# Optimization experiments

Hardware: AMD Instinct MI355X
Metric: run time of the kernel (lower is better)

Reference implementation:

```python
import jax, jax.numpy as jnp
import numpy as np

B, S = 8, 1024
D_MODEL = 1024
N_HEAD, HEAD_DIM = 16, 64
FIELD_W, FIELD_H = 32, 32  # S must equal FIELD_W * FIELD_H


def rotate_half(x):
    x1, x2 = jnp.split(x, 2, axis=-1)
    return jnp.concatenate((-x2, x1), axis=-1)


def apply_rope(q, k, cos, sin):
    # q,k: [B,S,H,D]; cos,sin: [S,D] -> broadcast over heads
    c = cos[:, None, :]
    s = sin[:, None, :]
    return q * c + rotate_half(q) * s, k * c + rotate_half(k) * s


def attention(q, k, v):
    # q,k,v: [B,S,H,D]; returns [B,S,H,D]
    scores = jnp.einsum('bqhd,bkhd->bhqk', q, k) * (HEAD_DIM ** -0.5)
    p = jax.nn.softmax(scores, axis=-1)
    return jnp.einsum('bhqk,bkhd->bqhd', p, v)


def setup_inputs() -> dict:
    key = jax.random.key(0)
    ks = jax.random.split(key, 5)
    hidden_states = jax.random.normal(ks[0], (B, S, D_MODEL), jnp.float32)
    cos = jax.random.uniform(ks[1], (S, HEAD_DIM), jnp.float32, minval=-1.0, maxval=1.0)
    sin = jax.random.uniform(ks[2], (S, HEAD_DIM), jnp.float32, minval=-1.0, maxval=1.0)
    w_qkv = jax.random.normal(ks[3], (3 * N_HEAD * HEAD_DIM, D_MODEL), jnp.float32) * (D_MODEL ** -0.5)
    w_o = jax.random.normal(ks[4], (D_MODEL, N_HEAD * HEAD_DIM), jnp.float32) * ((N_HEAD * HEAD_DIM) ** -0.5)
    return {"hidden_states": hidden_states, "cos": cos, "sin": sin, "w_qkv": w_qkv, "w_o": w_o}


def reference(hidden_states, cos, sin, w_qkv, w_o):
    b, s, _ = hidden_states.shape
    qkv = hidden_states @ w_qkv.T                       # [B,S,3*H*D]
    qkv = qkv.reshape(b, s, 3 * N_HEAD, HEAD_DIM)
    q = qkv[:, :, :N_HEAD]
    k = qkv[:, :, N_HEAD:2 * N_HEAD]
    v = qkv[:, :, 2 * N_HEAD:]
    # horizontal pass: standard RoPE
    q1, k1 = apply_rope(q, k, cos[:s], sin[:s])
    attn_out = attention(q1, k1, v)
    # vertical pass: transposed-field RoPE indexing
    idx = jnp.arange(FIELD_W * FIELD_H).reshape(FIELD_W, FIELD_H).T.reshape(-1)
    q2, k2 = apply_rope(q, k, cos[idx], sin[idx])
    attn_out_v = attention(q2, k2, v)
    attn_out = (attn_out + attn_out_v) * 0.5
    return attn_out.reshape(b, s, N_HEAD * HEAD_DIM) @ w_o.T
```

## Files before the change

kernel.cpp:

```cpp
#include <hip/hip_runtime.h>


typedef __attribute__((ext_vector_type(8))) short s16x8;
typedef __attribute__((ext_vector_type(4))) float f32x4;
typedef __attribute__((ext_vector_type(16))) float f32x16;
typedef unsigned short ushort_t;

__device__ __forceinline__ float bf2f(unsigned short u) {
    unsigned x = ((unsigned)u) << 16;
    return __builtin_bit_cast(float, x);
}
__device__ __forceinline__ unsigned short f2bf(float f) {
    unsigned u = __builtin_bit_cast(unsigned, f);
    unsigned r = (u + 0x7fffu + ((u >> 16) & 1u)) >> 16;
    return (unsigned short)r;
}
__device__ __forceinline__ f32x4 mfma16(s16x8 a, s16x8 b, f32x4 c) {
    return __builtin_amdgcn_mfma_f32_16x16x32_bf16(a, b, c, 0, 0, 0);
}
__device__ __forceinline__ f32x16 mfma32(s16x8 a, s16x8 b, f32x16 c) {
    return __builtin_amdgcn_mfma_f32_32x32x16_bf16(a, b, c, 0, 0, 0);
}
__device__ __forceinline__ void gload16(const ushort_t* g, ushort_t* lds) {
    __builtin_amdgcn_global_load_lds(
        (const __attribute__((address_space(1))) unsigned int*)g,
        (__attribute__((address_space(3))) unsigned int*)lds, 16, 0, 0);
}
__device__ __forceinline__ float4 ld4f(const float* p) { return *reinterpret_cast<const float4*>(p); }
__device__ __forceinline__ s16x8 ldg8(const ushort_t* p) { return *reinterpret_cast<const s16x8*>(p); }

__device__ __forceinline__ unsigned cvtpk(float lo, float hi) {
    unsigned r;
    asm("v_cvt_pk_bf16_f32 %0, %1, %2" : "=v"(r) : "v"(lo), "v"(hi));
    return r;
}
__device__ __forceinline__ void pl32swap(unsigned& a, unsigned& b, int hi) {
#if __has_builtin(__builtin_amdgcn_permlane32_swap)
    auto r = __builtin_amdgcn_permlane32_swap((int)a, (int)b, false, false);
    a = (unsigned)r[0]; b = (unsigned)r[1];
#else
    unsigned sa = (unsigned)__shfl_xor((int)a, 32);
    unsigned sb = (unsigned)__shfl_xor((int)b, 32);
    unsigned na = hi ? sb : a;
    unsigned nb = hi ? b : sa;
    a = na; b = nb;
#endif
}
__device__ __forceinline__ s16x8 frag4(unsigned w0, unsigned w1, unsigned w2, unsigned w3) {
    union { unsigned u[4]; s16x8 v; } t;
    t.u[0] = w0; t.u[1] = w1; t.u[2] = w2; t.u[3] = w3;
    return t.v;
}

__global__ __launch_bounds__(256) void conv_f32_bf16(const float* __restrict__ s,
                                                     ushort_t* __restrict__ d, int n8)
{
    int i = blockIdx.x * blockDim.x + threadIdx.x;
    const int str = gridDim.x * blockDim.x;
    for (; i < n8; i += str) {
        float4 a = ld4f(s + (size_t)i * 8);
        float4 b = ld4f(s + (size_t)i * 8 + 4);
        s16x8 o;
        o[0] = (short)f2bf(a.x); o[1] = (short)f2bf(a.y); o[2] = (short)f2bf(a.z); o[3] = (short)f2bf(a.w);
        o[4] = (short)f2bf(b.x); o[5] = (short)f2bf(b.y); o[6] = (short)f2bf(b.z); o[7] = (short)f2bf(b.w);
        *reinterpret_cast<s16x8*>(d + (size_t)i * 8) = o;
    }
}

__global__ __launch_bounds__(256) void avg_to_bf16(const float* __restrict__ a,
                                                   const float* __restrict__ b,
                                                   ushort_t* __restrict__ o, int n8)
{
    int i = blockIdx.x * blockDim.x + threadIdx.x;
    const int str = gridDim.x * blockDim.x;
    for (; i < n8; i += str) {
        float4 x0 = ld4f(a + (size_t)i * 8), x1 = ld4f(a + (size_t)i * 8 + 4);
        float4 y0 = ld4f(b + (size_t)i * 8), y1 = ld4f(b + (size_t)i * 8 + 4);
        s16x8 v;
        v[0] = (short)f2bf(0.5f * (x0.x + y0.x)); v[1] = (short)f2bf(0.5f * (x0.y + y0.y));
        v[2] = (short)f2bf(0.5f * (x0.z + y0.z)); v[3] = (short)f2bf(0.5f * (x0.w + y0.w));
        v[4] = (short)f2bf(0.5f * (x1.x + y1.x)); v[5] = (short)f2bf(0.5f * (x1.y + y1.y));
        v[6] = (short)f2bf(0.5f * (x1.z + y1.z)); v[7] = (short)f2bf(0.5f * (x1.w + y1.w));
        *reinterpret_cast<s16x8*>(o + (size_t)i * 8) = v;
    }
}

template<bool SPLIT_QKV>
__global__ __launch_bounds__(256) void gemm_mfma(const ushort_t* __restrict__ A,
                                                 const ushort_t* __restrict__ B,
                                                 void* __restrict__ C0, void* __restrict__ C1,
                                                 void* __restrict__ C2,
                                                 int M, int N, int K)
{
    __shared__ ushort_t As[128 * 64];
    __shared__ ushort_t Bs[128 * 64];
    const int tid = threadIdx.x, l = tid & 63, w = tid >> 6;
    const int lr = l & 15, lg = l >> 4;
    const int m0 = blockIdx.y * 128, n0 = blockIdx.x * 128;
    const int wr = w >> 1, wc = w & 1;

    int srow[4], scol[4];
#pragma unroll
    for (int i = 0; i < 4; ++i) {
        const int chunk = i * 4 + w;
        const int row = chunk * 8 + (l >> 3);
        srow[i] = row;
        scol[i] = ((l & 7) ^ (row & 7)) * 8;
    }

    f32x4 acc[4][4];
#pragma unroll
    for (int mi = 0; mi < 4; ++mi)
#pragma unroll
        for (int ni = 0; ni < 4; ++ni) acc[mi][ni] = (f32x4){0.f, 0.f, 0.f, 0.f};

    for (int k0 = 0; k0 < K; k0 += 64) {
        __syncthreads();
#pragma unroll
        for (int i = 0; i < 4; ++i) {
            gload16(A + (size_t)(m0 + srow[i]) * K + k0 + scol[i], &As[(i * 4 + w) * 512]);
            gload16(B + (size_t)(n0 + srow[i]) * K + k0 + scol[i], &Bs[(i * 4 + w) * 512]);
        }
        __syncthreads();
#pragma unroll
        for (int kf = 0; kf < 2; ++kf) {
            s16x8 af[4], bf[4];
#pragma unroll
            for (int mi = 0; mi < 4; ++mi) {
                const int row = wr * 64 + mi * 16 + lr;
                af[mi] = *reinterpret_cast<const s16x8*>(&As[row * 64 + (((kf * 4 + lg) ^ (row & 7)) << 3)]);
            }
#pragma unroll
            for (int ni = 0; ni < 4; ++ni) {
                const int row = wc * 64 + ni * 16 + lr;
                bf[ni] = *reinterpret_cast<const s16x8*>(&Bs[row * 64 + (((kf * 4 + lg) ^ (row & 7)) << 3)]);
            }
#pragma unroll
            for (int mi = 0; mi < 4; ++mi)
#pragma unroll
                for (int ni = 0; ni < 4; ++ni)
                    acc[mi][ni] = mfma16(af[mi], bf[ni], acc[mi][ni]);
        }
    }

    if (SPLIT_QKV) {
        ushort_t* Cb = (ushort_t*)(n0 < 1024 ? C0 : (n0 < 2048 ? C1 : C2));
        const int nbase = n0 & 1023;
#pragma unroll
        for (int mi = 0; mi < 4; ++mi)
#pragma unroll
            for (int q = 0; q < 4; ++q) {
                const int row = m0 + wr * 64 + mi * 16 + lg * 4 + q;
#pragma unroll
                for (int ni = 0; ni < 4; ++ni)
                    Cb[(size_t)row * 1024 + nbase + wc * 64 + ni * 16 + lr] = f2bf(acc[mi][ni][q]);
            }
    } else {
#pragma unroll
        for (int mi = 0; mi < 4; ++mi)
#pragma unroll
            for (int q = 0; q < 4; ++q) {
                const int row = m0 + wr * 64 + mi * 16 + lg * 4 + q;
#pragma unroll
                for (int ni = 0; ni < 4; ++ni)
                    ((float*)C0)[(size_t)row * N + n0 + wc * 64 + ni * 16 + lr] = acc[mi][ni][q];
            }
    }
}

__global__ __launch_bounds__(256) void rope_rearrange(
    const ushort_t* __restrict__ kb, const ushort_t* __restrict__ vb,
    const float* __restrict__ cosp, const float* __restrict__ sinp,
    ushort_t* __restrict__ Kr, ushort_t* __restrict__ Vt)
{
    __shared__ ushort_t Vs[64 * 65];
    const int tid = threadIdx.x;
    const int sblk = blockIdx.x, h = blockIdx.y, b = blockIdx.z;
    const int r = tid >> 2, c16 = (tid & 3) * 16;
    const int cc = c16 ^ 32;
    const float sg = (c16 < 32) ? -1.f : 1.f;
    const int s = sblk * 64 + r;

    const ushort_t* krow = kb + (size_t)(b * 1024 + s) * 1024 + h * 64;
    const ushort_t* vrow = vb + (size_t)(b * 1024 + s) * 1024 + h * 64;

    s16x8 kx0 = ldg8(krow + c16), kx1 = ldg8(krow + c16 + 8);
    s16x8 ky0 = ldg8(krow + cc),  ky1 = ldg8(krow + cc + 8);

#pragma unroll
    for (int var = 0; var < 2; ++var) {
        const int pos = var ? ((s & 31) * 32 + (s >> 5)) : s;
        const float* crow = cosp + (size_t)pos * 64 + c16;
        const float* srow = sinp + (size_t)pos * 64 + c16;
        ushort_t* kout = Kr + (((size_t)(var * 8 + b) * 16 + h) * 1024 + s) * 64 + c16;
        s16x8 o0, o1;
#pragma unroll
        for (int j = 0; j < 8; ++j) {
            o0[j] = (short)f2bf(bf2f((unsigned short)kx0[j]) * crow[j]
                     + sg * bf2f((unsigned short)ky0[j]) * srow[j]);
            o1[j] = (short)f2bf(bf2f((unsigned short)kx1[j]) * crow[j + 8]
                     + sg * bf2f((unsigned short)ky1[j]) * srow[j + 8]);
        }
        *reinterpret_cast<s16x8*>(kout) = o0;
        *reinterpret_cast<s16x8*>(kout + 8) = o1;
    }

    s16x8 v0 = ldg8(vrow + c16), v1 = ldg8(vrow + c16 + 8);
#pragma unroll
    for (int j = 0; j < 8; ++j) {
        Vs[r * 65 + c16 + j] = (ushort_t)v0[j];
        Vs[r * 65 + c16 + 8 + j] = (ushort_t)v1[j];
    }
    __syncthreads();
    {
        const int dd = tid >> 2, cs = (tid & 3) * 16;
        s16x8 t0, t1;
#pragma unroll
        for (int j = 0; j < 8; ++j) {
            t0[j] = (short)Vs[(cs + j) * 65 + dd];
            t1[j] = (short)Vs[(cs + 8 + j) * 65 + dd];
        }
        ushort_t* vout = Vt + ((size_t)(b * 16 + h) * 64 + dd) * 1024 + sblk * 64 + cs;
        *reinterpret_cast<s16x8*>(vout) = t0;
        *reinterpret_cast<s16x8*>(vout + 8) = t1;
    }
}

__global__ __launch_bounds__(256) void attn_mfma4(
    const ushort_t* __restrict__ qb,
    const ushort_t* __restrict__ Kr,
    const ushort_t* __restrict__ Vt,
    const float* __restrict__ cosp, const float* __restrict__ sinp,
    float* __restrict__ out0, float* __restrict__ out1)
{
    __shared__ ushort_t Qs[128 * 64];
    __shared__ ushort_t Ks[64 * 64];
    __shared__ ushort_t Vs[64 * 64];

    const int bi = blockIdx.x;
    const int qt = (bi >> 3) & 7;
    const int g = ((bi >> 6) << 3) | (bi & 7);
    const int h = g & 15, bz = g >> 4;
    const int b = bz >> 1, var = bz & 1;

    const int tid = threadIdx.x;
    const int l = tid & 63, wq = tid >> 6;
    const int l31 = l & 31, hi = l >> 5;
    const int s0 = qt * 128;

    {
        const int r = tid >> 1;
        const int half = tid & 1;
        const int c32 = half * 32, cco = 32 - c32;
        const float sg = half ? 1.f : -1.f;
        const int p = s0 + r;
        const int pos = var ? ((p & 31) * 32 + (p >> 5)) : p;
        const ushort_t* qrow = qb + (size_t)(b * 1024 + p) * 1024 + h * 64;
        const float* crow = cosp + (size_t)pos * 64 + c32;
        const float* srow = sinp + (size_t)pos * 64 + c32;
        constexpr float SCALE = 0.125f * 1.44269504f;
#pragma unroll
        for (int u = 0; u < 4; ++u) {
            s16x8 xv = ldg8(qrow + c32 + u * 8);
            s16x8 yv = ldg8(qrow + cco + u * 8);
            s16x8 ov;
#pragma unroll
            for (int j = 0; j < 8; ++j) {
                const int e = u * 8 + j;
                ov[j] = (short)f2bf((bf2f((unsigned short)xv[j]) * crow[e]
                         + sg * bf2f((unsigned short)yv[j]) * srow[e]) * SCALE);
            }
            const int slot = ((c32 >> 3) + u) ^ (r & 7);
            *reinterpret_cast<s16x8*>(&Qs[r * 64 + slot * 8]) = ov;
        }
    }
    __syncthreads();

    s16x8 qf[4];
    {
        const int qrow = wq * 32 + l31;
#pragma unroll
        for (int kc = 0; kc < 4; ++kc)
            qf[kc] = *reinterpret_cast<const s16x8*>(
                &Qs[qrow * 64 + (((2 * kc + hi) ^ (qrow & 7)) << 3)]);
    }

    float l_i = 0.f;
    f32x16 O0, O1;
#pragma unroll
    for (int r = 0; r < 16; ++r) { O0[r] = 0.f; O1[r] = 0.f; }

    const ushort_t* kr_base = Kr + ((size_t)(var * 8 + b) * 16 + h) * 65536;
    const ushort_t* vt_base = Vt + ((size_t)(b * 16 + h)) * 65536;
    const int lrow8 = l >> 3;
    const int scol = ((l & 7) ^ lrow8) * 8;

    for (int kt = 0; kt < 16; ++kt) {
        __syncthreads();
#pragma unroll
        for (int i = 0; i < 2; ++i) {
            const int chunk = wq * 2 + i;
            const int row = chunk * 8 + lrow8;
            gload16(kr_base + (size_t)kt * 4096 + row * 64 + scol, &Ks[chunk * 512]);
            gload16(vt_base + (size_t)row * 1024 + kt * 64 + scol, &Vs[chunk * 512]);
        }
        __syncthreads();

        f32x16 St0, St1;
#pragma unroll
        for (int r = 0; r < 16; ++r) { St0[r] = 0.f; St1[r] = 0.f; }
        const int kr0 = l31, kr1 = 32 + l31;
#pragma unroll
        for (int kc = 0; kc < 4; ++kc) {
            s16x8 kf0 = *reinterpret_cast<const s16x8*>(
                &Ks[kr0 * 64 + (((2 * kc + hi) ^ (kr0 & 7)) << 3)]);
            s16x8 kf1 = *reinterpret_cast<const s16x8*>(
                &Ks[kr1 * 64 + (((2 * kc + hi) ^ (kr1 & 7)) << 3)]);
            St0 = mfma32(kf0, qf[kc], St0);
            St1 = mfma32(kf1, qf[kc], St1);
        }

        float rs0 = 0.f, rs1 = 0.f;
#pragma unroll
        for (int r = 0; r < 16; ++r) { St0[r] = __builtin_amdgcn_exp2f(St0[r]); rs0 += St0[r]; }
#pragma unroll
        for (int r = 0; r < 16; ++r) { St1[r] = __builtin_amdgcn_exp2f(St1[r]); rs1 += St1[r]; }
        l_i += rs0 + rs1;

#pragma unroll
        for (int t = 0; t < 2; ++t) {
            unsigned w0, w1, w2, w3, w4, w5, w6, w7;
            if (t == 0) {
                w0 = cvtpk(St0[0], St0[1]);   w1 = cvtpk(St0[2], St0[3]);
                w2 = cvtpk(St0[4], St0[5]);   w3 = cvtpk(St0[6], St0[7]);
                w4 = cvtpk(St0[8], St0[9]);   w5 = cvtpk(St0[10], St0[11]);
                w6 = cvtpk(St0[12], St0[13]); w7 = cvtpk(St0[14], St0[15]);
            } else {
                w0 = cvtpk(St1[0], St1[1]);   w1 = cvtpk(St1[2], St1[3]);
                w2 = cvtpk(St1[4], St1[5]);   w3 = cvtpk(St1[6], St1[7]);
                w4 = cvtpk(St1[8], St1[9]);   w5 = cvtpk(St1[10], St1[11]);
                w6 = cvtpk(St1[12], St1[13]); w7 = cvtpk(St1[14], St1[15]);
            }
            pl32swap(w0, w2, hi);
            pl32swap(w1, w3, hi);
            pl32swap(w4, w6, hi);
            pl32swap(w5, w7, hi);
            const s16x8 pf0 = frag4(w0, w1, w2, w3);
            const s16x8 pf1 = frag4(w4, w5, w6, w7);
#pragma unroll
            for (int cc = 0; cc < 2; ++cc) {
                const int c = 2 * t + cc;
                const s16x8 pf = cc ? pf1 : pf0;
                const int vr0 = l31, vr1 = 32 + l31;
                s16x8 vf0 = *reinterpret_cast<const s16x8*>(
                    &Vs[vr0 * 64 + (((2 * c + hi) ^ (vr0 & 7)) << 3)]);
                s16x8 vf1 = *reinterpret_cast<const s16x8*>(
                    &Vs[vr1 * 64 + (((2 * c + hi) ^ (vr1 & 7)) << 3)]);
                O0 = mfma32(vf0, pf, O0);
                O1 = mfma32(vf1, pf, O1);
            }
        }
    }

    float* outp = var ? out1 : out0;
    const float inv = 1.f / (l_i + __shfl_xor(l_i, 32));
    const int qrow = s0 + wq * 32 + l31;
    float* orow = outp + (size_t)(b * 1024 + qrow) * 1024 + h * 64;
#pragma unroll
    for (int gq = 0; gq < 4; ++gq) {
        const int d0 = 8 * gq + 4 * hi;
        *reinterpret_cast<float4*>(orow + d0) =
            make_float4(O0[4 * gq] * inv, O0[4 * gq + 1] * inv, O0[4 * gq + 2] * inv, O0[4 * gq + 3] * inv);
        *reinterpret_cast<float4*>(orow + 32 + d0) =
            make_float4(O1[4 * gq] * inv, O1[4 * gq + 1] * inv, O1[4 * gq + 2] * inv, O1[4 * gq + 3] * inv);
    }
}

extern "C" void kernel_launch(void* const* d_in, const int* in_sizes, int n_in,
                              void* d_out, int out_size, void* d_ws, size_t ws_size,
                              hipStream_t stream) {
    const float* hidden = (const float*)d_in[0];
    const float* cosp   = (const float*)d_in[1];
    const float* sinp   = (const float*)d_in[2];
    const float* wqkv   = (const float*)d_in[3];
    const float* wo     = (const float*)d_in[4];
    float* out = (float*)d_out;

    char* wsb = (char*)d_ws;
    ushort_t* hb      = (ushort_t*)(wsb);
    ushort_t* wqkvb   = (ushort_t*)(wsb + (16ull << 20));
    ushort_t* wob     = (ushort_t*)(wsb + (22ull << 20));
    ushort_t* qb      = (ushort_t*)(wsb + (24ull << 20));
    ushort_t* kb      = (ushort_t*)(wsb + (40ull << 20));
    ushort_t* vb      = (ushort_t*)(wsb + (56ull << 20));
    float*    attn0   = (float*)   (wsb + (40ull << 20));
    ushort_t* Kr      = (ushort_t*)(wsb + (72ull << 20));
    ushort_t* Vt      = hb;
    ushort_t* attnavg = (ushort_t*)(wsb + (104ull << 20));

    conv_f32_bf16<<<2048, 256, 0, stream>>>(hidden, hb, 8192 * 1024 / 8);
    conv_f32_bf16<<<768,  256, 0, stream>>>(wqkv, wqkvb, 3072 * 1024 / 8);
    conv_f32_bf16<<<256,  256, 0, stream>>>(wo, wob, 1024 * 1024 / 8);

    gemm_mfma<true><<<dim3(24, 64), 256, 0, stream>>>(hb, wqkvb, qb, kb, vb, 8192, 3072, 1024);

    rope_rearrange<<<dim3(16, 16, 8), 256, 0, stream>>>(kb, vb, cosp, sinp, Kr, Vt);

    attn_mfma4<<<2048, 256, 0, stream>>>(qb, Kr, Vt, cosp, sinp, attn0, out);

    avg_to_bf16<<<2048, 256, 0, stream>>>(attn0, out, attnavg, 8192 * 1024 / 8);

    gemm_mfma<false><<<dim3(8, 64), 256, 0, stream>>>(attnavg, wob, out, nullptr, nullptr, 8192, 1024, 1024);
}
```

Measured before the change: 323.1 us.

## Fuse both RoPE attention variants per block and average into bf16 in-kernel

The attention kernel now processes both RoPE variants (horizontal and transposed) in one block, accumulating the two normalized outputs with a 0.5 weight and writing a single bf16 averaged tensor. This removes the two fp32 attention output writes, the separate averaging kernel and its reads. The three fp32-to-bf16 conversion launches are merged into one kernel. In exchange, the grid halves to 1024 blocks, each with twice the serial work, which lowers parallelism and keeps extra accumulator registers live.

Measured after the change: 378.9 us. 1.17x slower.

```diff
diff --git a/kernel.cpp b/kernel.cpp
--- a/kernel.cpp
+++ b/kernel.cpp
@@ -4,6 +4,7 @@
 typedef __attribute__((ext_vector_type(8))) short s16x8;
 typedef __attribute__((ext_vector_type(4))) float f32x4;
 typedef __attribute__((ext_vector_type(16))) float f32x16;
+typedef __attribute__((ext_vector_type(2))) unsigned u32x2;
 typedef unsigned short ushort_t;
 
 __device__ __forceinline__ float bf2f(unsigned short u) {
@@ -52,36 +53,25 @@
     return t.v;
 }
 
-__global__ __launch_bounds__(256) void conv_f32_bf16(const float* __restrict__ s,
-                                                     ushort_t* __restrict__ d, int n8)
+__global__ __launch_bounds__(256) void conv3(
+    const float* __restrict__ sA, ushort_t* __restrict__ dA, int nA,
+    const float* __restrict__ sB, ushort_t* __restrict__ dB, int nB,
+    const float* __restrict__ sC, ushort_t* __restrict__ dC, int nC)
 {
+    const int total = nA + nB + nC;
     int i = blockIdx.x * blockDim.x + threadIdx.x;
     const int str = gridDim.x * blockDim.x;
-    for (; i < n8; i += str) {
-        float4 a = ld4f(s + (size_t)i * 8);
-        float4 b = ld4f(s + (size_t)i * 8 + 4);
+    for (; i < total; i += str) {
+        const float* s; ushort_t* d; int off;
+        if (i < nA)           { s = sA; d = dA; off = i; }
+        else if (i < nA + nB) { s = sB; d = dB; off = i - nA; }
+        else                  { s = sC; d = dC; off = i - nA - nB; }
+        float4 a = ld4f(s + (size_t)off * 8);
+        float4 b = ld4f(s + (size_t)off * 8 + 4);
         s16x8 o;
         o[0] = (short)f2bf(a.x); o[1] = (short)f2bf(a.y); o[2] = (short)f2bf(a.z); o[3] = (short)f2bf(a.w);
         o[4] = (short)f2bf(b.x); o[5] = (short)f2bf(b.y); o[6] = (short)f2bf(b.z); o[7] = (short)f2bf(b.w);
-        *reinterpret_cast<s16x8*>(d + (size_t)i * 8) = o;
-    }
-}
-
-__global__ __launch_bounds__(256) void avg_to_bf16(const float* __restrict__ a,
-                                                   const float* __restrict__ b,
-                                                   ushort_t* __restrict__ o, int n8)
-{
-    int i = blockIdx.x * blockDim.x + threadIdx.x;
-    const int str = gridDim.x * blockDim.x;
-    for (; i < n8; i += str) {
-        float4 x0 = ld4f(a + (size_t)i * 8), x1 = ld4f(a + (size_t)i * 8 + 4);
-        float4 y0 = ld4f(b + (size_t)i * 8), y1 = ld4f(b + (size_t)i * 8 + 4);
-        s16x8 v;
-        v[0] = (short)f2bf(0.5f * (x0.x + y0.x)); v[1] = (short)f2bf(0.5f * (x0.y + y0.y));
-        v[2] = (short)f2bf(0.5f * (x0.z + y0.z)); v[3] = (short)f2bf(0.5f * (x0.w + y0.w));
-        v[4] = (short)f2bf(0.5f * (x1.x + y1.x)); v[5] = (short)f2bf(0.5f * (x1.y + y1.y));
-        v[6] = (short)f2bf(0.5f * (x1.z + y1.z)); v[7] = (short)f2bf(0.5f * (x1.w + y1.w));
-        *reinterpret_cast<s16x8*>(o + (size_t)i * 8) = v;
+        *reinterpret_cast<s16x8*>(d + (size_t)off * 8) = o;
     }
 }
 
@@ -226,12 +216,12 @@
     }
 }
 
-__global__ __launch_bounds__(256) void attn_mfma4(
+__global__ __launch_bounds__(256) void attn_mfma5(
     const ushort_t* __restrict__ qb,
     const ushort_t* __restrict__ Kr,
     const ushort_t* __restrict__ Vt,
     const float* __restrict__ cosp, const float* __restrict__ sinp,
-    float* __restrict__ out0, float* __restrict__ out1)
+    ushort_t* __restrict__ outavg)
 {
     __shared__ ushort_t Qs[128 * 64];
     __shared__ ushort_t Ks[64 * 64];
@@ -240,139 +230,150 @@
     const int bi = blockIdx.x;
     const int qt = (bi >> 3) & 7;
     const int g = ((bi >> 6) << 3) | (bi & 7);
-    const int h = g & 15, bz = g >> 4;
-    const int b = bz >> 1, var = bz & 1;
+    const int h = g & 15, b = g >> 4;
 
     const int tid = threadIdx.x;
     const int l = tid & 63, wq = tid >> 6;
     const int l31 = l & 31, hi = l >> 5;
     const int s0 = qt * 128;
 
-    {
-        const int r = tid >> 1;
-        const int half = tid & 1;
-        const int c32 = half * 32, cco = 32 - c32;
-        const float sg = half ? 1.f : -1.f;
-        const int p = s0 + r;
-        const int pos = var ? ((p & 31) * 32 + (p >> 5)) : p;
-        const ushort_t* qrow = qb + (size_t)(b * 1024 + p) * 1024 + h * 64;
-        const float* crow = cosp + (size_t)pos * 64 + c32;
-        const float* srow = sinp + (size_t)pos * 64 + c32;
-        constexpr float SCALE = 0.125f * 1.44269504f;
-#pragma unroll
-        for (int u = 0; u < 4; ++u) {
-            s16x8 xv = ldg8(qrow + c32 + u * 8);
-            s16x8 yv = ldg8(qrow + cco + u * 8);
-            s16x8 ov;
-#pragma unroll
-            for (int j = 0; j < 8; ++j) {
-                const int e = u * 8 + j;
-                ov[j] = (short)f2bf((bf2f((unsigned short)xv[j]) * crow[e]
-                         + sg * bf2f((unsigned short)yv[j]) * srow[e]) * SCALE);
-            }
-            const int slot = ((c32 >> 3) + u) ^ (r & 7);
-            *reinterpret_cast<s16x8*>(&Qs[r * 64 + slot * 8]) = ov;
-        }
-    }
-    __syncthreads();
-
-    s16x8 qf[4];
-    {
-        const int qrow = wq * 32 + l31;
-#pragma unroll
-        for (int kc = 0; kc < 4; ++kc)
-            qf[kc] = *reinterpret_cast<const s16x8*>(
-                &Qs[qrow * 64 + (((2 * kc + hi) ^ (qrow & 7)) << 3)]);
-    }
-
-    float l_i = 0.f;
-    f32x16 O0, O1;
-#pragma unroll
-    for (int r = 0; r < 16; ++r) { O0[r] = 0.f; O1[r] = 0.f; }
-
-    const ushort_t* kr_base = Kr + ((size_t)(var * 8 + b) * 16 + h) * 65536;
     const ushort_t* vt_base = Vt + ((size_t)(b * 16 + h)) * 65536;
     const int lrow8 = l >> 3;
     const int scol = ((l & 7) ^ lrow8) * 8;
 
-    for (int kt = 0; kt < 16; ++kt) {
+    f32x16 R0, R1;
+#pragma unroll
+    for (int r = 0; r < 16; ++r) { R0[r] = 0.f; R1[r] = 0.f; }
+
+    for (int var = 0; var < 2; ++var) {
+        {
+            const int r = tid >> 1;
+            const int half = tid & 1;
+            const int c32 = half * 32, cco = 32 - c32;
+            const float sg = half ? 1.f : -1.f;
+            const int p = s0 + r;
+            const int pos = var ? ((p & 31) * 32 + (p >> 5)) : p;
+            const ushort_t* qrow = qb + (size_t)(b * 1024 + p) * 1024 + h * 64;
+            const float* crow = cosp + (size_t)pos * 64 + c32;
+            const float* srow = sinp + (size_t)pos * 64 + c32;
+            constexpr float SCALE = 0.125f * 1.44269504f;
+#pragma unroll
+            for (int u = 0; u < 4; ++u) {
+                s16x8 xv = ldg8(qrow + c32 + u * 8);
+                s16x8 yv = ldg8(qrow + cco + u * 8);
+                s16x8 ov;
+#pragma unroll
+                for (int j = 0; j < 8; ++j) {
+                    const int e = u * 8 + j;
+                    ov[j] = (short)f2bf((bf2f((unsigned short)xv[j]) * crow[e]
+                             + sg * bf2f((unsigned short)yv[j]) * srow[e]) * SCALE);
+                }
+                const int slot = ((c32 >> 3) + u) ^ (r & 7);
+                *reinterpret_cast<s16x8*>(&Qs[r * 64 + slot * 8]) = ov;
+            }
+        }
         __syncthreads();
-#pragma unroll
-        for (int i = 0; i < 2; ++i) {
-            const int chunk = wq * 2 + i;
-            const int row = chunk * 8 + lrow8;
-            gload16(kr_base + (size_t)kt * 4096 + row * 64 + scol, &Ks[chunk * 512]);
-            gload16(vt_base + (size_t)row * 1024 + kt * 64 + scol, &Vs[chunk * 512]);
-        }
-        __syncthreads();
-
-        f32x16 St0, St1;
-#pragma unroll
-        for (int r = 0; r < 16; ++r) { St0[r] = 0.f; St1[r] = 0.f; }
-        const int kr0 = l31, kr1 = 32 + l31;
-#pragma unroll
-        for (int kc = 0; kc < 4; ++kc) {
-            s16x8 kf0 = *reinterpret_cast<const s16x8*>(
-                &Ks[kr0 * 64 + (((2 * kc + hi) ^ (kr0 & 7)) << 3)]);
-            s16x8 kf1 = *reinterpret_cast<const s16x8*>(
-                &Ks[kr1 * 64 + (((2 * kc + hi) ^ (kr1 & 7)) << 3)]);
-            St0 = mfma32(kf0, qf[kc], St0);
-            St1 = mfma32(kf1, qf[kc], St1);
-        }
-
-        float rs0 = 0.f, rs1 = 0.f;
-#pragma unroll
-        for (int r = 0; r < 16; ++r) { St0[r] = __builtin_amdgcn_exp2f(St0[r]); rs0 += St0[r]; }
-#pragma unroll
-        for (int r = 0; r < 16; ++r) { St1[r] = __builtin_amdgcn_exp2f(St1[r]); rs1 += St1[r]; }
-        l_i += rs0 + rs1;
-
-#pragma unroll
-        for (int t = 0; t < 2; ++t) {
-            unsigned w0, w1, w2, w3, w4, w5, w6, w7;
-            if (t == 0) {
-                w0 = cvtpk(St0[0], St0[1]);   w1 = cvtpk(St0[2], St0[3]);
-                w2 = cvtpk(St0[4], St0[5]);   w3 = cvtpk(St0[6], St0[7]);
-                w4 = cvtpk(St0[8], St0[9]);   w5 = cvtpk(St0[10], St0[11]);
-                w6 = cvtpk(St0[12], St0[13]); w7 = cvtpk(St0[14], St0[15]);
-            } else {
-                w0 = cvtpk(St1[0], St1[1]);   w1 = cvtpk(St1[2], St1[3]);
-                w2 = cvtpk(St1[4], St1[5]);   w3 = cvtpk(St1[6], St1[7]);
-                w4 = cvtpk(St1[8], St1[9]);   w5 = cvtpk(St1[10], St1[11]);
-                w6 = cvtpk(St1[12], St1[13]); w7 = cvtpk(St1[14], St1[15]);
-            }
-            pl32swap(w0, w2, hi);
-            pl32swap(w1, w3, hi);
-            pl32swap(w4, w6, hi);
-            pl32swap(w5, w7, hi);
-            const s16x8 pf0 = frag4(w0, w1, w2, w3);
-            const s16x8 pf1 = frag4(w4, w5, w6, w7);
-#pragma unroll
-            for (int cc = 0; cc < 2; ++cc) {
-                const int c = 2 * t + cc;
-                const s16x8 pf = cc ? pf1 : pf0;
-                const int vr0 = l31, vr1 = 32 + l31;
-                s16x8 vf0 = *reinterpret_cast<const s16x8*>(
-                    &Vs[vr0 * 64 + (((2 * c + hi) ^ (vr0 & 7)) << 3)]);
-                s16x8 vf1 = *reinterpret_cast<const s16x8*>(
-                    &Vs[vr1 * 64 + (((2 * c + hi) ^ (vr1 & 7)) << 3)]);
-                O0 = mfma32(vf0, pf, O0);
-                O1 = mfma32(vf1, pf, O1);
-            }
-        }
-    }
-
-    float* outp = var ? out1 : out0;
-    const float inv = 1.f / (l_i + __shfl_xor(l_i, 32));
+
+        s16x8 qf[4];
+        {
+            const int qrow = wq * 32 + l31;
+#pragma unroll
+            for (int kc = 0; kc < 4; ++kc)
+                qf[kc] = *reinterpret_cast<const s16x8*>(
+                    &Qs[qrow * 64 + (((2 * kc + hi) ^ (qrow & 7)) << 3)]);
+        }
+
+        float l_i = 0.f;
+        f32x16 O0, O1;
+#pragma unroll
+        for (int r = 0; r < 16; ++r) { O0[r] = 0.f; O1[r] = 0.f; }
+
+        const ushort_t* kr_base = Kr + ((size_t)(var * 8 + b) * 16 + h) * 65536;
+
+        for (int kt = 0; kt < 16; ++kt) {
+            __syncthreads();
+#pragma unroll
+            for (int i = 0; i < 2; ++i) {
+                const int chunk = wq * 2 + i;
+                const int row = chunk * 8 + lrow8;
+                gload16(kr_base + (size_t)kt * 4096 + row * 64 + scol, &Ks[chunk * 512]);
+                gload16(vt_base + (size_t)row * 1024 + kt * 64 + scol, &Vs[chunk * 512]);
+            }
+            __syncthreads();
+
+            f32x16 St0, St1;
+#pragma unroll
+            for (int r = 0; r < 16; ++r) { St0[r] = 0.f; St1[r] = 0.f; }
+            const int kr0 = l31, kr1 = 32 + l31;
+#pragma unroll
+            for (int kc = 0; kc < 4; ++kc) {
+                s16x8 kf0 = *reinterpret_cast<const s16x8*>(
+                    &Ks[kr0 * 64 + (((2 * kc + hi) ^ (kr0 & 7)) << 3)]);
+                s16x8 kf1 = *reinterpret_cast<const s16x8*>(
+                    &Ks[kr1 * 64 + (((2 * kc + hi) ^ (kr1 & 7)) << 3)]);
+                St0 = mfma32(kf0, qf[kc], St0);
+                St1 = mfma32(kf1, qf[kc], St1);
+            }
+
+            float rs0 = 0.f, rs1 = 0.f;
+#pragma unroll
+            for (int r = 0; r < 16; ++r) { St0[r] = __builtin_amdgcn_exp2f(St0[r]); rs0 += St0[r]; }
+#pragma unroll
+            for (int r = 0; r < 16; ++r) { St1[r] = __builtin_amdgcn_exp2f(St1[r]); rs1 += St1[r]; }
+            l_i += rs0 + rs1;
+
+#pragma unroll
+            for (int t = 0; t < 2; ++t) {
+                unsigned w0, w1, w2, w3, w4, w5, w6, w7;
+                if (t == 0) {
+                    w0 = cvtpk(St0[0], St0[1]);   w1 = cvtpk(St0[2], St0[3]);
+                    w2 = cvtpk(St0[4], St0[5]);   w3 = cvtpk(St0[6], St0[7]);
+                    w4 = cvtpk(St0[8], St0[9]);   w5 = cvtpk(St0[10], St0[11]);
+                    w6 = cvtpk(St0[12], St0[13]); w7 = cvtpk(St0[14], St0[15]);
+                } else {
+                    w0 = cvtpk(St1[0], St1[1]);   w1 = cvtpk(St1[2], St1[3]);
+                    w2 = cvtpk(St1[4], St1[5]);   w3 = cvtpk(St1[6], St1[7]);
+                    w4 = cvtpk(St1[8], St1[9]);   w5 = cvtpk(St1[10], St1[11]);
+                    w6 = cvtpk(St1[12], St1[13]); w7 = cvtpk(St1[14], St1[15]);
+                }
+                pl32swap(w0, w2, hi);
+                pl32swap(w1, w3, hi);
+                pl32swap(w4, w6, hi);
+                pl32swap(w5, w7, hi);
+                const s16x8 pf0 = frag4(w0, w1, w2, w3);
+                const s16x8 pf1 = frag4(w4, w5, w6, w7);
+#pragma unroll
+                for (int cc = 0; cc < 2; ++cc) {
+                    const int c = 2 * t + cc;
+                    const s16x8 pf = cc ? pf1 : pf0;
+                    const int vr0 = l31, vr1 = 32 + l31;
+                    s16x8 vf0 = *reinterpret_cast<const s16x8*>(
+                        &Vs[vr0 * 64 + (((2 * c + hi) ^ (vr0 & 7)) << 3)]);
+                    s16x8 vf1 = *reinterpret_cast<const s16x8*>(
+                        &Vs[vr1 * 64 + (((2 * c + hi) ^ (vr1 & 7)) << 3)]);
+                    O0 = mfma32(vf0, pf, O0);
+                    O1 = mfma32(vf1, pf, O1);
+                }
+            }
+        }
+
+        const float inv = 0.5f / (l_i + __shfl_xor(l_i, 32));
+#pragma unroll
+        for (int r = 0; r < 16; ++r) { R0[r] += O0[r] * inv; R1[r] += O1[r] * inv; }
+    }
+
     const int qrow = s0 + wq * 32 + l31;
-    float* orow = outp + (size_t)(b * 1024 + qrow) * 1024 + h * 64;
+    ushort_t* orow = outavg + (size_t)(b * 1024 + qrow) * 1024 + h * 64;
 #pragma unroll
     for (int gq = 0; gq < 4; ++gq) {
         const int d0 = 8 * gq + 4 * hi;
-        *reinterpret_cast<float4*>(orow + d0) =
-            make_float4(O0[4 * gq] * inv, O0[4 * gq + 1] * inv, O0[4 * gq + 2] * inv, O0[4 * gq + 3] * inv);
-        *reinterpret_cast<float4*>(orow + 32 + d0) =
-            make_float4(O1[4 * gq] * inv, O1[4 * gq + 1] * inv, O1[4 * gq + 2] * inv, O1[4 * gq + 3] * inv);
+        u32x2 pa, pb;
+        pa[0] = cvtpk(R0[4 * gq], R0[4 * gq + 1]);
+        pa[1] = cvtpk(R0[4 * gq + 2], R0[4 * gq + 3]);
+        pb[0] = cvtpk(R1[4 * gq], R1[4 * gq + 1]);
+        pb[1] = cvtpk(R1[4 * gq + 2], R1[4 * gq + 3]);
+        *reinterpret_cast<u32x2*>(orow + d0) = pa;
+        *reinterpret_cast<u32x2*>(orow + 32 + d0) = pb;
     }
 }
 
@@ -393,22 +394,19 @@
     ushort_t* qb      = (ushort_t*)(wsb + (24ull << 20));
     ushort_t* kb      = (ushort_t*)(wsb + (40ull << 20));
     ushort_t* vb      = (ushort_t*)(wsb + (56ull << 20));
-    float*    attn0   = (float*)   (wsb + (40ull << 20));
     ushort_t* Kr      = (ushort_t*)(wsb + (72ull << 20));
     ushort_t* Vt      = hb;
-    ushort_t* attnavg = (ushort_t*)(wsb + (104ull << 20));
-
-    conv_f32_bf16<<<2048, 256, 0, stream>>>(hidden, hb, 8192 * 1024 / 8);
-    conv_f32_bf16<<<768,  256, 0, stream>>>(wqkv, wqkvb, 3072 * 1024 / 8);
-    conv_f32_bf16<<<256,  256, 0, stream>>>(wo, wob, 1024 * 1024 / 8);
+    ushort_t* attnavg = kb;
+
+    conv3<<<1536, 256, 0, stream>>>(hidden, hb, 8192 * 1024 / 8,
+                                    wqkv, wqkvb, 3072 * 1024 / 8,
+                                    wo, wob, 1024 * 1024 / 8);
 
     gemm_mfma<true><<<dim3(24, 64), 256, 0, stream>>>(hb, wqkvb, qb, kb, vb, 8192, 3072, 1024);
 
     rope_rearrange<<<dim3(16, 16, 8), 256, 0, stream>>>(kb, vb, cosp, sinp, Kr, Vt);
 
-    attn_mfma4<<<2048, 256, 0, stream>>>(qb, Kr, Vt, cosp, sinp, attn0, out);
-
-    avg_to_bf16<<<2048, 256, 0, stream>>>(attn0, out, attnavg, 8192 * 1024 / 8);
+    attn_mfma5<<<1024, 256, 0, stream>>>(qb, Kr, Vt, cosp, sinp, attnavg);
 
     gemm_mfma<false><<<dim3(8, 64), 256, 0, stream>>>(attnavg, wob, out, nullptr, nullptr, 8192, 1024, 1024);
 }
```

## Store K/V in fragment-blocked layout and merge conversion kernels into one launch

Applied to the files above, without the earlier changes.

The rope/rearrange kernel now writes rotated K and transposed V in a blocked layout of 8-element column groups by row within each 64-row tile. The attention kernel can then load tiles with contiguous global_load_lds and read MFMA fragments from LDS without XOR swizzling, and Q in LDS uses the same layout. Separately, the three fp32-to-bf16 conversion launches are merged into one kernel to cut launch overhead. The unswizzled LDS reads may cause bank conflicts, which could offset part of the gain from the contiguous loads.

Measured after the change: 321.6 us. About the same (-0.5%).

```diff
diff --git a/kernel.cpp b/kernel.cpp
--- a/kernel.cpp
+++ b/kernel.cpp
@@ -52,18 +52,25 @@
     return t.v;
 }
 
-__global__ __launch_bounds__(256) void conv_f32_bf16(const float* __restrict__ s,
-                                                     ushort_t* __restrict__ d, int n8)
+__global__ __launch_bounds__(256) void conv3(
+    const float* __restrict__ sA, ushort_t* __restrict__ dA, int nA,
+    const float* __restrict__ sB, ushort_t* __restrict__ dB, int nB,
+    const float* __restrict__ sC, ushort_t* __restrict__ dC, int nC)
 {
+    const int total = nA + nB + nC;
     int i = blockIdx.x * blockDim.x + threadIdx.x;
     const int str = gridDim.x * blockDim.x;
-    for (; i < n8; i += str) {
-        float4 a = ld4f(s + (size_t)i * 8);
-        float4 b = ld4f(s + (size_t)i * 8 + 4);
+    for (; i < total; i += str) {
+        const float* s; ushort_t* d; int off;
+        if (i < nA)           { s = sA; d = dA; off = i; }
+        else if (i < nA + nB) { s = sB; d = dB; off = i - nA; }
+        else                  { s = sC; d = dC; off = i - nA - nB; }
+        float4 a = ld4f(s + (size_t)off * 8);
+        float4 b = ld4f(s + (size_t)off * 8 + 4);
         s16x8 o;
         o[0] = (short)f2bf(a.x); o[1] = (short)f2bf(a.y); o[2] = (short)f2bf(a.z); o[3] = (short)f2bf(a.w);
         o[4] = (short)f2bf(b.x); o[5] = (short)f2bf(b.y); o[6] = (short)f2bf(b.z); o[7] = (short)f2bf(b.w);
-        *reinterpret_cast<s16x8*>(d + (size_t)i * 8) = o;
+        *reinterpret_cast<s16x8*>(d + (size_t)off * 8) = o;
     }
 }
 
@@ -192,7 +199,8 @@
         const int pos = var ? ((s & 31) * 32 + (s >> 5)) : s;
         const float* crow = cosp + (size_t)pos * 64 + c16;
         const float* srow = sinp + (size_t)pos * 64 + c16;
-        ushort_t* kout = Kr + (((size_t)(var * 8 + b) * 16 + h) * 1024 + s) * 64 + c16;
+        ushort_t* kout = Kr + (((size_t)(var * 8 + b) * 16 + h) * 65536)
+                            + (size_t)sblk * 4096 + (c16 >> 3) * 512 + r * 8;
         s16x8 o0, o1;
 #pragma unroll
         for (int j = 0; j < 8; ++j) {
@@ -202,7 +210,7 @@
                      + sg * bf2f((unsigned short)ky1[j]) * srow[j + 8]);
         }
         *reinterpret_cast<s16x8*>(kout) = o0;
-        *reinterpret_cast<s16x8*>(kout + 8) = o1;
+        *reinterpret_cast<s16x8*>(kout + 512) = o1;
     }
 
     s16x8 v0 = ldg8(vrow + c16), v1 = ldg8(vrow + c16 + 8);
@@ -220,13 +228,14 @@
             t0[j] = (short)Vs[(cs + j) * 65 + dd];
             t1[j] = (short)Vs[(cs + 8 + j) * 65 + dd];
         }
-        ushort_t* vout = Vt + ((size_t)(b * 16 + h) * 64 + dd) * 1024 + sblk * 64 + cs;
+        ushort_t* vout = Vt + ((size_t)(b * 16 + h) * 65536)
+                            + (size_t)sblk * 4096 + (cs >> 3) * 512 + dd * 8;
         *reinterpret_cast<s16x8*>(vout) = t0;
-        *reinterpret_cast<s16x8*>(vout + 8) = t1;
-    }
-}
-
-__global__ __launch_bounds__(256) void attn_mfma4(
+        *reinterpret_cast<s16x8*>(vout + 512) = t1;
+    }
+}
+
+__global__ __launch_bounds__(256) void attn_mfma6(
     const ushort_t* __restrict__ qb,
     const ushort_t* __restrict__ Kr,
     const ushort_t* __restrict__ Vt,
@@ -270,8 +279,7 @@
                 ov[j] = (short)f2bf((bf2f((unsigned short)xv[j]) * crow[e]
                          + sg * bf2f((unsigned short)yv[j]) * srow[e]) * SCALE);
             }
-            const int slot = ((c32 >> 3) + u) ^ (r & 7);
-            *reinterpret_cast<s16x8*>(&Qs[r * 64 + slot * 8]) = ov;
+            *reinterpret_cast<s16x8*>(&Qs[((half * 4 + u) * 128 + r) * 8]) = ov;
         }
     }
     __syncthreads();
@@ -281,8 +289,7 @@
         const int qrow = wq * 32 + l31;
 #pragma unroll
         for (int kc = 0; kc < 4; ++kc)
-            qf[kc] = *reinterpret_cast<const s16x8*>(
-                &Qs[qrow * 64 + (((2 * kc + hi) ^ (qrow & 7)) << 3)]);
+            qf[kc] = *reinterpret_cast<const s16x8*>(&Qs[((2 * kc + hi) * 128 + qrow) * 8]);
     }
 
     float l_i = 0.f;
@@ -292,30 +299,25 @@
 
     const ushort_t* kr_base = Kr + ((size_t)(var * 8 + b) * 16 + h) * 65536;
     const ushort_t* vt_base = Vt + ((size_t)(b * 16 + h)) * 65536;
-    const int lrow8 = l >> 3;
-    const int scol = ((l & 7) ^ lrow8) * 8;
 
     for (int kt = 0; kt < 16; ++kt) {
         __syncthreads();
 #pragma unroll
         for (int i = 0; i < 2; ++i) {
             const int chunk = wq * 2 + i;
-            const int row = chunk * 8 + lrow8;
-            gload16(kr_base + (size_t)kt * 4096 + row * 64 + scol, &Ks[chunk * 512]);
-            gload16(vt_base + (size_t)row * 1024 + kt * 64 + scol, &Vs[chunk * 512]);
+            gload16(kr_base + (size_t)kt * 4096 + chunk * 512 + l * 8, &Ks[chunk * 512]);
+            gload16(vt_base + (size_t)kt * 4096 + chunk * 512 + l * 8, &Vs[chunk * 512]);
         }
         __syncthreads();
 
         f32x16 St0, St1;
 #pragma unroll
         for (int r = 0; r < 16; ++r) { St0[r] = 0.f; St1[r] = 0.f; }
-        const int kr0 = l31, kr1 = 32 + l31;
 #pragma unroll
         for (int kc = 0; kc < 4; ++kc) {
-            s16x8 kf0 = *reinterpret_cast<const s16x8*>(
-                &Ks[kr0 * 64 + (((2 * kc + hi) ^ (kr0 & 7)) << 3)]);
-            s16x8 kf1 = *reinterpret_cast<const s16x8*>(
-                &Ks[kr1 * 64 + (((2 * kc + hi) ^ (kr1 & 7)) << 3)]);
+            const int d8 = 2 * kc + hi;
+            s16x8 kf0 = *reinterpret_cast<const s16x8*>(&Ks[d8 * 512 + l31 * 8]);
+            s16x8 kf1 = *reinterpret_cast<const s16x8*>(&Ks[d8 * 512 + (32 + l31) * 8]);
             St0 = mfma32(kf0, qf[kc], St0);
             St1 = mfma32(kf1, qf[kc], St1);
         }
@@ -349,13 +351,10 @@
             const s16x8 pf1 = frag4(w4, w5, w6, w7);
 #pragma unroll
             for (int cc = 0; cc < 2; ++cc) {
-                const int c = 2 * t + cc;
+                const int sg8 = 2 * (2 * t + cc) + hi;
                 const s16x8 pf = cc ? pf1 : pf0;
-                const int vr0 = l31, vr1 = 32 + l31;
-                s16x8 vf0 = *reinterpret_cast<const s16x8*>(
-                    &Vs[vr0 * 64 + (((2 * c + hi) ^ (vr0 & 7)) << 3)]);
-                s16x8 vf1 = *reinterpret_cast<const s16x8*>(
-                    &Vs[vr1 * 64 + (((2 * c + hi) ^ (vr1 & 7)) << 3)]);
+                s16x8 vf0 = *reinterpret_cast<const s16x8*>(&Vs[sg8 * 512 + l31 * 8]);
+                s16x8 vf1 = *reinterpret_cast<const s16x8*>(&Vs[sg8 * 512 + (32 + l31) * 8]);
                 O0 = mfma32(vf0, pf, O0);
                 O1 = mfma32(vf1, pf, O1);
             }
@@ -398,15 +397,15 @@
     ushort_t* Vt      = hb;
     ushort_t* attnavg = (ushort_t*)(wsb + (104ull << 20));
 
-    conv_f32_bf16<<<2048, 256, 0, stream>>>(hidden, hb, 8192 * 1024 / 8);
-    conv_f32_bf16<<<768,  256, 0, stream>>>(wqkv, wqkvb, 3072 * 1024 / 8);
-    conv_f32_bf16<<<256,  256, 0, stream>>>(wo, wob, 1024 * 1024 / 8);
+    conv3<<<1536, 256, 0, stream>>>(hidden, hb, 8192 * 1024 / 8,
+                                    wqkv, wqkvb, 3072 * 1024 / 8,
+                                    wo, wob, 1024 * 1024 / 8);
 
     gemm_mfma<true><<<dim3(24, 64), 256, 0, stream>>>(hb, wqkvb, qb, kb, vb, 8192, 3072, 1024);
 
     rope_rearrange<<<dim3(16, 16, 8), 256, 0, stream>>>(kb, vb, cosp, sinp, Kr, Vt);
 
-    attn_mfma4<<<2048, 256, 0, stream>>>(qb, Kr, Vt, cosp, sinp, attn0, out);
+    attn_mfma6<<<2048, 256, 0, stream>>>(qb, Kr, Vt, cosp, sinp, attn0, out);
 
     avg_to_bf16<<<2048, 256, 0, stream>>>(attn0, out, attnavg, 8192 * 1024 / 8);
 
```
